# Performance work log

Hardware: AMD Instinct MI355X
Metric: run time of the kernel (lower is better)

## Reference

```python
import jax, jax.numpy as jnp
import numpy as np

N, E, IN, H = 50000, 800000, 128, 64
BN_EPS = 1e-5


def _bn(x, g, b, m, v):
    return (x - m) * jax.lax.rsqrt(v + BN_EPS) * g + b


def _gat(x, src, dst, W, a_s, a_d, bias):
    # PyG GATConv (heads=1): project, per-edge attention with self-loops,
    # segment softmax over destination, scatter-weighted aggregation.
    h = x @ W                                  # [N, H]
    as_n = h @ a_s                             # [N]
    ad_n = h @ a_d                             # [N]
    e = jax.nn.leaky_relu(as_n[src] + ad_n[dst], 0.2)   # [E+N]
    emax = jax.ops.segment_max(e, dst, num_segments=N)
    ex = jnp.exp(e - emax[dst])
    denom = jax.ops.segment_sum(ex, dst, num_segments=N)
    alpha = ex / (denom[dst] + 1e-16)
    out = jax.ops.segment_sum(alpha[:, None] * h[src], dst, num_segments=N)
    return out + bias


def setup_inputs() -> dict:
    key = jax.random.key(0)
    ks = jax.random.split(key, 24)
    inp = {}
    inp['x'] = jax.random.normal(ks[0], (N, IN), dtype=jnp.float32)
    inp['edge_index'] = jax.random.randint(ks[1], (2, E), 0, N, dtype=jnp.int32)
    s = 0.1
    inp['conv1_W'] = jax.random.normal(ks[2], (IN, H)) * s
    inp['conv1_as'] = jax.random.normal(ks[3], (H,)) * s
    inp['conv1_ad'] = jax.random.normal(ks[4], (H,)) * s
    inp['conv1_b'] = jnp.zeros((H,))
    inp['convW'] = jax.random.normal(ks[5], (4, H, H)) * s
    inp['conv_as'] = jax.random.normal(ks[6], (4, H)) * s
    inp['conv_ad'] = jax.random.normal(ks[7], (4, H)) * s
    inp['conv_b'] = jnp.zeros((4, H))
    inp['bn_g'] = jnp.ones((5, H))
    inp['bn_b'] = jnp.zeros((5, H))
    inp['bn_m'] = jax.random.normal(ks[8], (5, H)) * 0.01
    inp['bn_v'] = jnp.ones((5, H))
    inp['projW'] = jax.random.normal(ks[9], (4, H, H)) * s
    inp['projb'] = jnp.zeros((4, H))
    inp['hW1'] = jax.random.normal(ks[10], (H, H // 2)) * s
    inp['hb1'] = jnp.zeros((H // 2,))
    inp['hbn_g'] = jnp.ones((H // 2,))
    inp['hbn_b'] = jnp.zeros((H // 2,))
    inp['hbn_m'] = jax.random.normal(ks[11], (H // 2,)) * 0.01
    inp['hbn_v'] = jnp.ones((H // 2,))
    inp['hW2'] = jax.random.normal(ks[12], (H // 2, 1)) * s
    inp['hb2'] = jnp.zeros((1,))
    return inp


def reference(x, edge_index, conv1_W, conv1_as, conv1_ad, conv1_b, convW, conv_as, conv_ad, conv_b, bn_g, bn_b, bn_m, bn_v, projW, projb, hW1, hb1, hbn_g, hbn_b, hbn_m, hbn_v, hW2, hb2):
    loop = jnp.arange(N, dtype=edge_index.dtype)
    src = jnp.concatenate([edge_index[0], loop])  # self-loops (PyG default)
    dst = jnp.concatenate([edge_index[1], loop])

    x1 = jax.nn.relu(_gat(x, src, dst, conv1_W, conv1_as, conv1_ad, conv1_b))
    x1 = _bn(x1, bn_g[0], bn_b[0], bn_m[0], bn_v[0])

    xp = x1
    for l in range(4):  # conv2..conv5 (dropout identity in eval)
        xc = jax.nn.relu(_gat(xp, src, dst, convW[l], conv_as[l], conv_ad[l], conv_b[l]))
        xc = _bn(xc, bn_g[l + 1], bn_b[l + 1], bn_m[l + 1], bn_v[l + 1]) + (xp @ projW[l] + projb[l])
        xp = xc

    g = jnp.mean(xp, axis=0, keepdims=True)      # global_mean_pool, single graph -> [1, H]
    h1 = jax.nn.relu(g @ hW1 + hb1)
    h1 = _bn(h1, hbn_g, hbn_b, hbn_m, hbn_v)
    out = (h1 @ hW2 + hb2).squeeze(-1)           # [1]
    return out
```

## Files before the change

### kernel.cpp

```cpp
#include <hip/hip_runtime.h>
#include <hip/hip_bf16.h>

#define N_NODES 50000
#define N_EDGES 800000
#define EN_EDGES (N_EDGES + N_NODES)
#define IN_F 128
#define H_F 64
#define BN_EPS 1e-5f
#define SCAN_NB 49
#define POOL_NB 256


__global__ void k_init(int* __restrict__ cursor) {
    int i = blockIdx.x * 256 + threadIdx.x;
    if (i < N_NODES) cursor[i] = 1;
}

__global__ void k_hist(const int* __restrict__ dst, int* __restrict__ cursor) {
    int e = blockIdx.x * 256 + threadIdx.x;
    if (e < N_EDGES) atomicAdd(&cursor[dst[e]], 1);
}

__global__ void k_scan_bsum(const int* __restrict__ cnt, int* __restrict__ bsum) {
    __shared__ int sd[256];
    int b = blockIdx.x, t = threadIdx.x;
    int base = b * 1024;
    int s = 0;
    for (int i = t; i < 1024; i += 256) {
        int idx = base + i;
        if (idx < N_NODES) s += cnt[idx];
    }
    sd[t] = s; __syncthreads();
    for (int d = 128; d > 0; d >>= 1) {
        if (t < d) sd[t] += sd[t + d];
        __syncthreads();
    }
    if (t == 0) bsum[b] = sd[0];
}

__global__ void k_scan_small(int* __restrict__ bsum, int* __restrict__ offsets) {
    if (threadIdx.x == 0 && blockIdx.x == 0) {
        int run = 0;
        for (int i = 0; i < SCAN_NB; i++) { int v = bsum[i]; bsum[i] = run; run += v; }
        offsets[N_NODES] = run;
    }
}

__global__ void k_scan_final(int* __restrict__ cntcur, const int* __restrict__ bsum,
                             int* __restrict__ offsets) {
    __shared__ int ls[256];
    int b = blockIdx.x, t = threadIdx.x;
    int i0 = b * 1024 + t * 4;
    int c0 = 0, c1 = 0, c2 = 0, c3 = 0;
    if (i0 + 0 < N_NODES) c0 = cntcur[i0 + 0];
    if (i0 + 1 < N_NODES) c1 = cntcur[i0 + 1];
    if (i0 + 2 < N_NODES) c2 = cntcur[i0 + 2];
    if (i0 + 3 < N_NODES) c3 = cntcur[i0 + 3];
    int tsum = c0 + c1 + c2 + c3;
    ls[t] = tsum; __syncthreads();
    for (int d = 1; d < 256; d <<= 1) {
        int v = (t >= d) ? ls[t - d] : 0;
        __syncthreads();
        ls[t] += v;
        __syncthreads();
    }
    int tex = ls[t] - tsum;
    int base = bsum[b] + tex;
    if (i0 + 0 < N_NODES) { offsets[i0 + 0] = base; cntcur[i0 + 0] = base; base += c0; }
    if (i0 + 1 < N_NODES) { offsets[i0 + 1] = base; cntcur[i0 + 1] = base; base += c1; }
    if (i0 + 2 < N_NODES) { offsets[i0 + 2] = base; cntcur[i0 + 2] = base; base += c2; }
    if (i0 + 3 < N_NODES) { offsets[i0 + 3] = base; cntcur[i0 + 3] = base; base += c3; }
}

__global__ void k_scatter(const int* __restrict__ src, const int* __restrict__ dst,
                          int* __restrict__ cursor, int* __restrict__ ssrc) {
    int e = blockIdx.x * 256 + threadIdx.x;
    if (e >= EN_EDGES) return;
    int s, d;
    if (e < N_EDGES) { s = src[e]; d = dst[e]; }
    else { s = e - N_EDGES; d = s; }
    int pos = atomicAdd(&cursor[d], 1);
    ssrc[pos] = s;
}

__global__ __launch_bounds__(256) void k_gemm1(
        const float* __restrict__ x, const float* __restrict__ W,
        const float* __restrict__ a_s, const float* __restrict__ a_d,
        float* __restrict__ h, float* __restrict__ asn, float* __restrict__ adn) {
    __shared__ float Xs[64 * 129];
    __shared__ float asb[4][64], adb[4][64];
    int t = threadIdx.x, lane = t & 63, wave = t >> 6;
    int row0 = blockIdx.x * 64;
    for (int i = t; i < 64 * IN_F; i += 256) {
        int r = i >> 7, c = i & 127;
        Xs[r * 129 + c] = (row0 + r < N_NODES) ? x[(size_t)(row0 + r) * IN_F + c] : 0.f;
    }
    __syncthreads();
    int jb = __builtin_amdgcn_readfirstlane(wave << 4);
    float acc[16];
    #pragma unroll
    for (int j = 0; j < 16; j++) acc[j] = 0.f;
    for (int k0 = 0; k0 < IN_F; k0 += 8) {
        float xr[8];
        #pragma unroll
        for (int kk = 0; kk < 8; kk++) xr[kk] = Xs[lane * 129 + k0 + kk];
        #pragma unroll
        for (int kk = 0; kk < 8; kk++) {
            const float* wr = W + (k0 + kk) * H_F + jb;
            #pragma unroll
            for (int j = 0; j < 16; j++) acc[j] = fmaf(xr[kk], wr[j], acc[j]);
        }
    }
    int row = row0 + lane;
    float pa = 0.f, pd = 0.f;
    #pragma unroll
    for (int j = 0; j < 16; j++) { pa += acc[j] * a_s[jb + j]; pd += acc[j] * a_d[jb + j]; }
    asb[wave][lane] = pa; adb[wave][lane] = pd;
    if (row < N_NODES) {
        float4* hp = (float4*)(h + (size_t)row * H_F + jb);
        #pragma unroll
        for (int q = 0; q < 4; q++)
            hp[q] = make_float4(acc[4*q], acc[4*q+1], acc[4*q+2], acc[4*q+3]);
    }
    __syncthreads();
    if (wave == 0 && row < N_NODES) {
        asn[row] = asb[0][lane] + asb[1][lane] + asb[2][lane] + asb[3][lane];
        adn[row] = adb[0][lane] + adb[1][lane] + adb[2][lane] + adb[3][lane];
    }
}

__global__ __launch_bounds__(256) void k_gemm(
        const float* __restrict__ xp, const float* __restrict__ W,
        const float* __restrict__ PW, const float* __restrict__ pbias,
        const float* __restrict__ a_s, const float* __restrict__ a_d,
        float* __restrict__ h, float* __restrict__ p,
        float* __restrict__ asn, float* __restrict__ adn) {
    __shared__ float Xs[64 * 65];
    __shared__ float asb[4][64], adb[4][64];
    int t = threadIdx.x, lane = t & 63, wave = t >> 6;
    int row0 = blockIdx.x * 64;
    for (int i = t; i < 64 * H_F; i += 256) {
        int r = i >> 6, c = i & 63;
        Xs[r * 65 + c] = (row0 + r < N_NODES) ? xp[(size_t)(row0 + r) * H_F + c] : 0.f;
    }
    __syncthreads();
    int jb = __builtin_amdgcn_readfirstlane(wave << 4);
    float acc[16], pac[16];
    #pragma unroll
    for (int j = 0; j < 16; j++) { acc[j] = 0.f; pac[j] = 0.f; }
    for (int k0 = 0; k0 < H_F; k0 += 8) {
        float xr[8];
        #pragma unroll
        for (int kk = 0; kk < 8; kk++) xr[kk] = Xs[lane * 65 + k0 + kk];
        #pragma unroll
        for (int kk = 0; kk < 8; kk++) {
            const float* wr = W  + (k0 + kk) * H_F + jb;
            const float* pr = PW + (k0 + kk) * H_F + jb;
            #pragma unroll
            for (int j = 0; j < 16; j++) {
                acc[j] = fmaf(xr[kk], wr[j], acc[j]);
                pac[j] = fmaf(xr[kk], pr[j], pac[j]);
            }
        }
    }
    int row = row0 + lane;
    float pa = 0.f, pd = 0.f;
    #pragma unroll
    for (int j = 0; j < 16; j++) { pa += acc[j] * a_s[jb + j]; pd += acc[j] * a_d[jb + j]; }
    asb[wave][lane] = pa; adb[wave][lane] = pd;
    if (row < N_NODES) {
        float4* hp = (float4*)(h + (size_t)row * H_F + jb);
        float4* pp = (float4*)(p + (size_t)row * H_F + jb);
        #pragma unroll
        for (int q = 0; q < 4; q++) {
            hp[q] = make_float4(acc[4*q], acc[4*q+1], acc[4*q+2], acc[4*q+3]);
            pp[q] = make_float4(pac[4*q] + pbias[jb+4*q],   pac[4*q+1] + pbias[jb+4*q+1],
                                pac[4*q+2] + pbias[jb+4*q+2], pac[4*q+3] + pbias[jb+4*q+3]);
        }
    }
    __syncthreads();
    if (wave == 0 && row < N_NODES) {
        asn[row] = asb[0][lane] + asb[1][lane] + asb[2][lane] + asb[3][lane];
        adn[row] = adb[0][lane] + adb[1][lane] + adb[2][lane] + adb[3][lane];
    }
}

template <bool HAS_RES>
__global__ __launch_bounds__(256) void k_attn_aggr(
        const float* __restrict__ h, const float* __restrict__ asn, const float* __restrict__ adn,
        const int* __restrict__ offsets, const int* __restrict__ ssrc,
        const float* __restrict__ bias,
        const float* __restrict__ bg, const float* __restrict__ bb,
        const float* __restrict__ bm, const float* __restrict__ bv,
        const float* __restrict__ res, float* __restrict__ out) {
    int t = threadIdx.x, lane = t & 63, wave = t >> 6;
    int d = blockIdx.x * 4 + wave;
    if (d >= N_NODES) return;
    int du  = __builtin_amdgcn_readfirstlane(d);
    int beg = __builtin_amdgcn_readfirstlane(offsets[du]);
    int end = __builtin_amdgcn_readfirstlane(offsets[du + 1]);
    float add = adn[du];

    float m = -1e30f, ssum = 0.f;
    for (int j = beg + lane; j < end; j += 64) {
        float e = asn[ssrc[j]] + add;
        e = e < 0.f ? 0.2f * e : e;
        float nm = fmaxf(m, e);
        ssum = ssum * __expf(m - nm) + __expf(e - nm);
        m = nm;
    }
    #pragma unroll
    for (int dlt = 32; dlt > 0; dlt >>= 1) {
        float m2 = __shfl_xor(m, dlt);
        float s2 = __shfl_xor(ssum, dlt);
        float nm = fmaxf(m, m2);
        ssum = ssum * __expf(m - nm) + s2 * __expf(m2 - nm);
        m = nm;
    }
    float inv = 1.f / ssum;

    float acc = 0.f;
    #pragma unroll 4
    for (int e = beg; e < end; ++e) {
        int s    = ssrc[e];
        float ev = asn[s] + add;
        ev = ev < 0.f ? 0.2f * ev : ev;
        float a  = __expf(ev - m) * inv;
        acc = fmaf(a, h[(size_t)s * H_F + lane], acc);
    }

    float v = acc + bias[lane];
    v = fmaxf(v, 0.f);
    v = (v - bm[lane]) * rsqrtf(bv[lane] + BN_EPS) * bg[lane] + bb[lane];
    if (HAS_RES) v += res[(size_t)d * H_F + lane];
    out[(size_t)d * H_F + lane] = v;
}

__global__ __launch_bounds__(256) void k_pool(const float* __restrict__ x,
                                              float* __restrict__ partials) {
    __shared__ float red[256 * 4];
    int t = threadIdx.x, b = blockIdx.x;
    const float4* xv = (const float4*)x;
    const int total = N_NODES * (H_F / 4);
    float a0 = 0.f, a1 = 0.f, a2 = 0.f, a3 = 0.f;
    for (int i = b * 256 + t; i < total; i += POOL_NB * 256) {
        float4 v = xv[i];
        a0 += v.x; a1 += v.y; a2 += v.z; a3 += v.w;
    }
    red[t * 4 + 0] = a0; red[t * 4 + 1] = a1; red[t * 4 + 2] = a2; red[t * 4 + 3] = a3;
    __syncthreads();
    if (t < 64) {
        int p = t >> 2, q = t & 3;
        float s = 0.f;
        #pragma unroll
        for (int k = 0; k < 16; k++) s += red[(p + 16 * k) * 4 + q];
        partials[b * H_F + t] = s;
    }
}

__global__ __launch_bounds__(256) void k_head(
        const float* __restrict__ partials,
        const float* __restrict__ hW1, const float* __restrict__ hb1,
        const float* __restrict__ hg, const float* __restrict__ hb,
        const float* __restrict__ hm, const float* __restrict__ hv,
        const float* __restrict__ hW2, const float* __restrict__ hb2,
        float* __restrict__ out) {
    __shared__ float red[256];
    __shared__ float gl[64];
    __shared__ float h1[32];
    int t = threadIdx.x;
    int f = t & 63, g = t >> 6;
    float s = 0.f;
    for (int k = g; k < POOL_NB; k += 4) s += partials[k * H_F + f];
    red[t] = s;
    __syncthreads();
    if (t < 64) gl[t] = (red[t] + red[64 + t] + red[128 + t] + red[192 + t]) * (1.f / N_NODES);
    __syncthreads();
    if (t < 32) {
        float v = hb1[t];
        for (int l = 0; l < 64; l++) v += gl[l] * hW1[l * 32 + t];
        v = fmaxf(v, 0.f);
        v = (v - hm[t]) * rsqrtf(hv[t] + BN_EPS) * hg[t] + hb[t];
        h1[t] = v;
    }
    __syncthreads();
    if (t == 0) {
        float v = hb2[0];
        for (int j = 0; j < 32; j++) v += h1[j] * hW2[j];
        out[0] = v;
    }
}


extern "C" void kernel_launch(void* const* d_in, const int* in_sizes, int n_in,
                              void* d_out, int out_size, void* d_ws, size_t ws_size,
                              hipStream_t stream) {
    (void)in_sizes; (void)n_in; (void)out_size; (void)ws_size;
    const float* x        = (const float*)d_in[0];
    const int*   ei       = (const int*)d_in[1];
    const float* conv1_W  = (const float*)d_in[2];
    const float* conv1_as = (const float*)d_in[3];
    const float* conv1_ad = (const float*)d_in[4];
    const float* conv1_b  = (const float*)d_in[5];
    const float* convW    = (const float*)d_in[6];
    const float* conv_as  = (const float*)d_in[7];
    const float* conv_ad  = (const float*)d_in[8];
    const float* conv_b   = (const float*)d_in[9];
    const float* bn_g     = (const float*)d_in[10];
    const float* bn_b     = (const float*)d_in[11];
    const float* bn_m     = (const float*)d_in[12];
    const float* bn_v     = (const float*)d_in[13];
    const float* projW    = (const float*)d_in[14];
    const float* projb    = (const float*)d_in[15];
    const float* hW1      = (const float*)d_in[16];
    const float* hb1      = (const float*)d_in[17];
    const float* hbn_g    = (const float*)d_in[18];
    const float* hbn_b    = (const float*)d_in[19];
    const float* hbn_m    = (const float*)d_in[20];
    const float* hbn_v    = (const float*)d_in[21];
    const float* hW2      = (const float*)d_in[22];
    const float* hb2      = (const float*)d_in[23];

    const int* e_src = ei;
    const int* e_dst = ei + N_EDGES;

    char* wsb = (char*)d_ws;
    size_t cur = 0;
    auto alloc = [&](size_t bytes) -> void* {
        void* p = wsb + cur;
        cur = (cur + bytes + 255) & ~(size_t)255;
        return p;
    };
    int*   offsets  = (int*)alloc((N_NODES + 1) * sizeof(int));
    int*   cursor   = (int*)alloc(N_NODES * sizeof(int));
    int*   ssrc     = (int*)alloc(EN_EDGES * sizeof(int));
    int*   bsum     = (int*)alloc(64 * sizeof(int));
    float* h        = (float*)alloc((size_t)N_NODES * H_F * sizeof(float));
    float* p        = (float*)alloc((size_t)N_NODES * H_F * sizeof(float));
    float* asn      = (float*)alloc(N_NODES * sizeof(float));
    float* adn      = (float*)alloc(N_NODES * sizeof(float));
    float* xa       = (float*)alloc((size_t)N_NODES * H_F * sizeof(float));
    float* xb       = (float*)alloc((size_t)N_NODES * H_F * sizeof(float));
    float* partials = (float*)alloc(POOL_NB * H_F * sizeof(float));

    k_init<<<dim3((N_NODES + 255) / 256), dim3(256), 0, stream>>>(cursor);
    k_hist<<<dim3((N_EDGES + 255) / 256), dim3(256), 0, stream>>>(e_dst, cursor);
    k_scan_bsum<<<dim3(SCAN_NB), dim3(256), 0, stream>>>(cursor, bsum);
    k_scan_small<<<dim3(1), dim3(64), 0, stream>>>(bsum, offsets);
    k_scan_final<<<dim3(SCAN_NB), dim3(256), 0, stream>>>(cursor, bsum, offsets);
    k_scatter<<<dim3((EN_EDGES + 255) / 256), dim3(256), 0, stream>>>(e_src, e_dst, cursor, ssrc);

    dim3 blk(256);
    dim3 gemm_grid((N_NODES + 63) / 64);
    dim3 aggr_grid((N_NODES + 3) / 4);

    k_gemm1<<<gemm_grid, blk, 0, stream>>>(x, conv1_W, conv1_as, conv1_ad, h, asn, adn);
    k_attn_aggr<false><<<aggr_grid, blk, 0, stream>>>(h, asn, adn, offsets, ssrc, conv1_b,
                                                      bn_g, bn_b, bn_m, bn_v, nullptr, xa);

    float* bufs[2] = { xa, xb };
    for (int l = 0; l < 4; l++) {
        float* in  = bufs[l & 1];
        float* out = bufs[(l + 1) & 1];
        k_gemm<<<gemm_grid, blk, 0, stream>>>(in, convW + (size_t)l * H_F * H_F,
                                              projW + (size_t)l * H_F * H_F, projb + l * H_F,
                                              conv_as + l * H_F, conv_ad + l * H_F,
                                              h, p, asn, adn);
        k_attn_aggr<true><<<aggr_grid, blk, 0, stream>>>(h, asn, adn, offsets, ssrc,
                                                         conv_b + l * H_F,
                                                         bn_g + (l + 1) * H_F, bn_b + (l + 1) * H_F,
                                                         bn_m + (l + 1) * H_F, bn_v + (l + 1) * H_F,
                                                         p, out);
    }

    k_pool<<<dim3(POOL_NB), blk, 0, stream>>>(xa, partials);
    k_head<<<dim3(1), blk, 0, stream>>>(partials, hW1, hb1, hbn_g, hbn_b, hbn_m, hbn_v,
                                        hW2, hb2, (float*)d_out);
}
```

Measured before the change: 565.5 us.

## Single-pass edge-parallel GAT aggregation, fuse scatter with first GEMM, vectorize histogram

The attention aggregation becomes a single pass. Each wave works on 4 edges at once, with 16 lanes per edge doing float4 gathers, accumulating unnormalized exp weights and reducing across groups with shuffles. This drops the separate max/sum pass and the one-edge-at-a-time scalar feature loop. The CSR scatter and the first projection GEMM now run in one launch with disjoint block ranges. The histogram reads four destinations per thread with an int4 load. The softmax no longer subtracts the per-segment max, so large attention logits could overflow exp.

After: 586.9 us. 1.04x slower.

```diff
diff --git a/kernel.cpp b/kernel.cpp
--- a/kernel.cpp
+++ b/kernel.cpp
@@ -9,6 +9,8 @@
 #define BN_EPS 1e-5f
 #define SCAN_NB 49
 #define POOL_NB 256
+#define SCAT_NB ((EN_EDGES + 255) / 256)
+#define GEMM1_NB ((N_NODES + 63) / 64)
 
 
 __global__ void k_init(int* __restrict__ cursor) {
@@ -17,8 +19,17 @@
 }
 
 __global__ void k_hist(const int* __restrict__ dst, int* __restrict__ cursor) {
-    int e = blockIdx.x * 256 + threadIdx.x;
-    if (e < N_EDGES) atomicAdd(&cursor[dst[e]], 1);
+    int i = blockIdx.x * 256 + threadIdx.x;
+    int e = i * 4;
+    if (e + 3 < N_EDGES) {
+        int4 d4 = *(const int4*)(dst + e);
+        atomicAdd(&cursor[d4.x], 1);
+        atomicAdd(&cursor[d4.y], 1);
+        atomicAdd(&cursor[d4.z], 1);
+        atomicAdd(&cursor[d4.w], 1);
+    } else {
+        for (int k = e; k < N_EDGES; k++) atomicAdd(&cursor[dst[k]], 1);
+    }
 }
 
 __global__ void k_scan_bsum(const int* __restrict__ cnt, int* __restrict__ bsum) {
@@ -72,25 +83,29 @@
     if (i0 + 3 < N_NODES) { offsets[i0 + 3] = base; cntcur[i0 + 3] = base; base += c3; }
 }
 
-__global__ void k_scatter(const int* __restrict__ src, const int* __restrict__ dst,
-                          int* __restrict__ cursor, int* __restrict__ ssrc) {
-    int e = blockIdx.x * 256 + threadIdx.x;
-    if (e >= EN_EDGES) return;
-    int s, d;
-    if (e < N_EDGES) { s = src[e]; d = dst[e]; }
-    else { s = e - N_EDGES; d = s; }
-    int pos = atomicAdd(&cursor[d], 1);
-    ssrc[pos] = s;
-}
-
-__global__ __launch_bounds__(256) void k_gemm1(
+__global__ __launch_bounds__(256) void k_scatter_gemm1(
+        const int* __restrict__ src, const int* __restrict__ dst,
+        int* __restrict__ cursor, int* __restrict__ ssrc,
         const float* __restrict__ x, const float* __restrict__ W,
         const float* __restrict__ a_s, const float* __restrict__ a_d,
         float* __restrict__ h, float* __restrict__ asn, float* __restrict__ adn) {
     __shared__ float Xs[64 * 129];
     __shared__ float asb[4][64], adb[4][64];
-    int t = threadIdx.x, lane = t & 63, wave = t >> 6;
-    int row0 = blockIdx.x * 64;
+    int t = threadIdx.x;
+
+    if (blockIdx.x < SCAT_NB) {
+        int e = blockIdx.x * 256 + t;
+        if (e >= EN_EDGES) return;
+        int s, d;
+        if (e < N_EDGES) { s = src[e]; d = dst[e]; }
+        else { s = e - N_EDGES; d = s; }
+        int pos = atomicAdd(&cursor[d], 1);
+        ssrc[pos] = s;
+        return;
+    }
+
+    int lane = t & 63, wave = t >> 6;
+    int row0 = (blockIdx.x - SCAT_NB) * 64;
     for (int i = t; i < 64 * IN_F; i += 256) {
         int r = i >> 7, c = i & 127;
         Xs[r * 129 + c] = (row0 + r < N_NODES) ? x[(size_t)(row0 + r) * IN_F + c] : 0.f;
@@ -200,40 +215,58 @@
     int beg = __builtin_amdgcn_readfirstlane(offsets[du]);
     int end = __builtin_amdgcn_readfirstlane(offsets[du + 1]);
     float add = adn[du];
-
-    float m = -1e30f, ssum = 0.f;
-    for (int j = beg + lane; j < end; j += 64) {
-        float e = asn[ssrc[j]] + add;
-        e = e < 0.f ? 0.2f * e : e;
-        float nm = fmaxf(m, e);
-        ssum = ssum * __expf(m - nm) + __expf(e - nm);
-        m = nm;
-    }
-    #pragma unroll
-    for (int dlt = 32; dlt > 0; dlt >>= 1) {
-        float m2 = __shfl_xor(m, dlt);
-        float s2 = __shfl_xor(ssum, dlt);
-        float nm = fmaxf(m, m2);
-        ssum = ssum * __expf(m - nm) + s2 * __expf(m2 - nm);
-        m = nm;
-    }
-    float inv = 1.f / ssum;
-
-    float acc = 0.f;
-    #pragma unroll 4
-    for (int e = beg; e < end; ++e) {
-        int s    = ssrc[e];
+    int grp = lane >> 4, fl = lane & 15;
+    int last = end - 1;
+
+    float4 acc = make_float4(0.f, 0.f, 0.f, 0.f);
+    float ssum = 0.f;
+    #pragma unroll 2
+    for (int e0 = beg; e0 < end; e0 += 4) {
+        int e = e0 + grp;
+        bool valid = e < end;
+        e = valid ? e : last;
+        int s = ssrc[e];
         float ev = asn[s] + add;
         ev = ev < 0.f ? 0.2f * ev : ev;
-        float a  = __expf(ev - m) * inv;
-        acc = fmaf(a, h[(size_t)s * H_F + lane], acc);
-    }
-
-    float v = acc + bias[lane];
-    v = fmaxf(v, 0.f);
-    v = (v - bm[lane]) * rsqrtf(bv[lane] + BN_EPS) * bg[lane] + bb[lane];
-    if (HAS_RES) v += res[(size_t)d * H_F + lane];
-    out[(size_t)d * H_F + lane] = v;
+        float w = valid ? __expf(ev) : 0.f;
+        const float4* hp = (const float4*)(h + (size_t)s * H_F);
+        float4 hv = hp[fl];
+        ssum += w;
+        acc.x = fmaf(w, hv.x, acc.x);
+        acc.y = fmaf(w, hv.y, acc.y);
+        acc.z = fmaf(w, hv.z, acc.z);
+        acc.w = fmaf(w, hv.w, acc.w);
+    }
+    #pragma unroll
+    for (int dlt = 16; dlt < 64; dlt <<= 1) {
+        acc.x += __shfl_xor(acc.x, dlt);
+        acc.y += __shfl_xor(acc.y, dlt);
+        acc.z += __shfl_xor(acc.z, dlt);
+        acc.w += __shfl_xor(acc.w, dlt);
+        ssum  += __shfl_xor(ssum,  dlt);
+    }
+    if (lane < 16) {
+        float inv = 1.f / (ssum + 1e-16f);
+        float4 b4 = ((const float4*)bias)[fl];
+        float4 g4 = ((const float4*)bg)[fl];
+        float4 o4 = ((const float4*)bb)[fl];
+        float4 m4 = ((const float4*)bm)[fl];
+        float4 v4 = ((const float4*)bv)[fl];
+        float4 o;
+        o.x = fmaxf(fmaf(acc.x, inv, b4.x), 0.f);
+        o.y = fmaxf(fmaf(acc.y, inv, b4.y), 0.f);
+        o.z = fmaxf(fmaf(acc.z, inv, b4.z), 0.f);
+        o.w = fmaxf(fmaf(acc.w, inv, b4.w), 0.f);
+        o.x = (o.x - m4.x) * rsqrtf(v4.x + BN_EPS) * g4.x + o4.x;
+        o.y = (o.y - m4.y) * rsqrtf(v4.y + BN_EPS) * g4.y + o4.y;
+        o.z = (o.z - m4.z) * rsqrtf(v4.z + BN_EPS) * g4.z + o4.z;
+        o.w = (o.w - m4.w) * rsqrtf(v4.w + BN_EPS) * g4.w + o4.w;
+        if (HAS_RES) {
+            float4 r = ((const float4*)(res + (size_t)d * H_F))[fl];
+            o.x += r.x; o.y += r.y; o.z += r.z; o.w += r.w;
+        }
+        ((float4*)(out + (size_t)d * H_F))[fl] = o;
+    }
 }
 
 __global__ __launch_bounds__(256) void k_pool(const float* __restrict__ x,
@@ -343,18 +376,20 @@
     float* xb       = (float*)alloc((size_t)N_NODES * H_F * sizeof(float));
     float* partials = (float*)alloc(POOL_NB * H_F * sizeof(float));
 
-    k_init<<<dim3((N_NODES + 255) / 256), dim3(256), 0, stream>>>(cursor);
-    k_hist<<<dim3((N_EDGES + 255) / 256), dim3(256), 0, stream>>>(e_dst, cursor);
-    k_scan_bsum<<<dim3(SCAN_NB), dim3(256), 0, stream>>>(cursor, bsum);
+    dim3 blk(256);
+
+    k_init<<<dim3((N_NODES + 255) / 256), blk, 0, stream>>>(cursor);
+    k_hist<<<dim3((N_EDGES / 4 + 255) / 256), blk, 0, stream>>>(e_dst, cursor);
+    k_scan_bsum<<<dim3(SCAN_NB), blk, 0, stream>>>(cursor, bsum);
     k_scan_small<<<dim3(1), dim3(64), 0, stream>>>(bsum, offsets);
-    k_scan_final<<<dim3(SCAN_NB), dim3(256), 0, stream>>>(cursor, bsum, offsets);
-    k_scatter<<<dim3((EN_EDGES + 255) / 256), dim3(256), 0, stream>>>(e_src, e_dst, cursor, ssrc);
-
-    dim3 blk(256);
+    k_scan_final<<<dim3(SCAN_NB), blk, 0, stream>>>(cursor, bsum, offsets);
+
+    k_scatter_gemm1<<<dim3(SCAT_NB + GEMM1_NB), blk, 0, stream>>>(
+        e_src, e_dst, cursor, ssrc, x, conv1_W, conv1_as, conv1_ad, h, asn, adn);
+
     dim3 gemm_grid((N_NODES + 63) / 64);
     dim3 aggr_grid((N_NODES + 3) / 4);
 
-    k_gemm1<<<gemm_grid, blk, 0, stream>>>(x, conv1_W, conv1_as, conv1_ad, h, asn, adn);
     k_attn_aggr<false><<<aggr_grid, blk, 0, stream>>>(h, asn, adn, offsets, ssrc, conv1_b,
                                                       bn_g, bn_b, bn_m, bn_v, nullptr, xa);
 
```
